# Optimization experiments

Measured on AMD Instinct MI355X. Metric: run time of the kernel, lower is better.

Reference implementation:

```python
import jax, jax.numpy as jnp
import numpy as np

N = 1024        # graph nodes
B = 64          # batch
F_IN = 128
F_OUT = 128
DEG = 8         # avg degree of the random adjacency
NEG = -9.0e15   # mask fill value used by the original module


def _make_masks():
    rng = np.random.default_rng(0)
    a = rng.random((N, N)) < (DEG / N)
    a = np.triu(a, 1)
    adj = (a | a.T).astype(np.float32)          # symmetric, no self loops
    m0 = np.eye(N, dtype=bool)                  # adj_0 = I
    m1 = adj > 0                                # adj_1 = adj
    a2 = adj @ adj
    m2 = a2 > 0                                 # adj_2 = adj @ adj
    a3 = a2 @ adj
    m3 = a3 > 0                                 # adj_3 = adj_2 @ adj
    return m0, m1, m2, m3


def setup_inputs() -> dict:
    key = jax.random.key(0)
    ks = jax.random.split(key, 8)
    m0, m1, m2, m3 = _make_masks()
    return {
        "x": jax.random.normal(ks[0], (B, N, F_IN), dtype=jnp.float32),
        "W": jax.random.normal(ks[1], (4, F_IN, F_OUT), dtype=jnp.float32) * 0.1,
        "E0": jax.random.normal(ks[2], (N, N), dtype=jnp.float32),
        "E1": jax.random.normal(ks[3], (N, N), dtype=jnp.float32),
        "E2": jax.random.normal(ks[4], (N, N), dtype=jnp.float32),
        "E3": jax.random.normal(ks[5], (N, N), dtype=jnp.float32),
        "bias": jax.random.normal(ks[6], (4 * F_OUT,), dtype=jnp.float32) * 0.05,
        "m0": jnp.asarray(m0),
        "m1": jnp.asarray(m1),
        "m2": jnp.asarray(m2),
        "m3": jnp.asarray(m3),
    }


def reference(x, W, E0, E1, E2, E3, bias, m0, m1, m2, m3):
    def hop(E, m, Wk):
        h = jnp.einsum('bnf,fo->bno', x, Wk)                  # [B,N,F_OUT]
        A = jax.nn.softmax(jnp.where(m, E, NEG), axis=1)      # row-softmax over masked scores
        return jnp.einsum('ij,bjo->bio', A, h)                # [B,N,F_OUT]

    out0 = hop(E0, m0, W[0])
    out1 = hop(E1, m1, W[1])
    out2 = hop(E2, m2, W[2])
    out3 = hop(E3, m3, W[3])
    out = jnp.concatenate([out0, out1, out2, out3], axis=2)   # [B,N,4*F_OUT]
    return out + bias[None, None, :]
```

## Files before the change

kernel.cpp:

```cpp
#include <hip/hip_runtime.h>
#include <cstdint>
#include <cstddef>


#define NODES 1024
#define BATCH 64
#define FDIM  128

typedef __attribute__((ext_vector_type(8)))  short  short8;
typedef __attribute__((ext_vector_type(4)))  float  floatx4;
typedef __attribute__((ext_vector_type(16))) float  floatx16;

__device__ __forceinline__ unsigned short f2bf(float f) {
  union { float f; unsigned int u; } v; v.f = f;
  unsigned int r = v.u + 0x7fffu + ((v.u >> 16) & 1u);
  return (unsigned short)(r >> 16);
}

__device__ __forceinline__ void async_copy16(const void* g, void* l) {
  __builtin_amdgcn_global_load_lds(
      (const __attribute__((address_space(1))) void*)g,
      (__attribute__((address_space(3))) void*)l, 16, 0, 0);
}

__device__ __forceinline__ void wg_barrier() {
  asm volatile("" ::: "memory");
  __builtin_amdgcn_s_barrier();
  asm volatile("" ::: "memory");
}

__global__ __launch_bounds__(256) void prep(
    const float* __restrict__ E1, const float* __restrict__ E2, const float* __restrict__ E3,
    const void* __restrict__ m1v, const void* __restrict__ m2v, const void* __restrict__ m3v,
    const void* __restrict__ m0v, unsigned short* __restrict__ Aout,
    const float* __restrict__ W, unsigned short* __restrict__ Wt) {
  const int row = blockIdx.x, hop = blockIdx.y;
  const int tid = threadIdx.x;

  if (hop == 3) {
    if (row < 256) {
      const int idx = row * 256 + tid;
      const int k = idx >> 14, rem = idx & 16383;
      const int f = rem >> 7, o = rem & 127;
      Wt[(k << 14) + o * 128 + f] = f2bf(W[idx]);
    }
    return;
  }

  const int lane = tid & 63, wave = tid >> 6;
  const float* E  = (hop == 0) ? E1 : (hop == 1) ? E2 : E3;
  const void* mv  = (hop == 0) ? m1v : (hop == 1) ? m2v : m3v;
  const bool bytelay = (((const int*)m0v)[256] != 0);

  float v[4]; bool mk[4];
#pragma unroll
  for (int i = 0; i < 4; ++i) {
    const int j = tid + i * 256;
    const size_t e = (size_t)row * NODES + j;
    const bool m = bytelay ? (((const unsigned char*)mv)[e] != 0)
                           : (((const int*)mv)[e] != 0);
    mk[i] = m;
    v[i] = m ? E[e] : -__builtin_inff();
  }
  float mx = fmaxf(fmaxf(v[0], v[1]), fmaxf(v[2], v[3]));
#pragma unroll
  for (int off = 32; off > 0; off >>= 1) mx = fmaxf(mx, __shfl_down(mx, off));
  __shared__ float rm[4], rs[4];
  if (lane == 0) rm[wave] = mx;
  __syncthreads();
  mx = fmaxf(fmaxf(rm[0], rm[1]), fmaxf(rm[2], rm[3]));

  float ex[4], s = 0.f;
#pragma unroll
  for (int i = 0; i < 4; ++i) {
    ex[i] = mk[i] ? __expf(v[i] - mx) : 0.f;
    s += ex[i];
  }
#pragma unroll
  for (int off = 32; off > 0; off >>= 1) s += __shfl_down(s, off);
  if (lane == 0) rs[wave] = s;
  __syncthreads();
  s = rs[0] + rs[1] + rs[2] + rs[3];

  const bool uni = (mx == -__builtin_inff());
  const float inv = uni ? 0.f : 1.f / s;
  unsigned short* dst = Aout + (size_t)hop * NODES * NODES + (size_t)row * NODES;
#pragma unroll
  for (int i = 0; i < 4; ++i) {
    const float val = uni ? (1.f / 1024.f) : ex[i] * inv;
    dst[tid + i * 256] = f2bf(val);
  }
}

__global__ __launch_bounds__(256) void h_gemm(
    const float* __restrict__ x, const unsigned short* __restrict__ Wt,
    const float* __restrict__ bias, unsigned short* __restrict__ Ht,
    float* __restrict__ out) {
  __shared__ unsigned short sX[128 * 128];
  __shared__ unsigned short sW[128 * 128];
  const int jt = blockIdx.x, b = blockIdx.y;
  const int tid = threadIdx.x, lane = tid & 63, wave = tid >> 6;
  const int ln = lane & 15, q = lane >> 4;
  const int p = ln & 7;
  const int j0 = jt * 128;

#pragma unroll
  for (int t = 0; t < 16; ++t) {
    const int g = tid + t * 256;
    const int row = g >> 5, c4 = (g & 31) * 4;
    const float4 vv = *(const float4*)(x + ((size_t)b * NODES + j0 + row) * FDIM + c4);
    ushort4 u;
    u.x = f2bf(vv.x); u.y = f2bf(vv.y); u.z = f2bf(vv.z); u.w = f2bf(vv.w);
    const int col8 = c4 >> 3, off = c4 & 7;
    const int p8 = (col8 & 8) | ((col8 ^ (row & 7)) & 7);
    *(ushort4*)(&sX[row * 128 + p8 * 8 + off]) = u;
  }

  for (int kz = 0; kz < 4; ++kz) {
#pragma unroll
    for (int t = 0; t < 8; ++t) {
      const int gi = wave * 512 + t * 64 + lane;
      const int row = gi >> 4, kb = gi & 15;
      const int src8 = ((kb & 8) | ((kb ^ (row & 7)) & 7)) * 8;
      async_copy16(Wt + (kz << 14) + row * 128 + src8,
                   (char*)sW + (size_t)(wave * 512 + t * 64) * 16);
    }
    __syncthreads();

    const unsigned short* aT = (kz == 0) ? sX : sW;
    const unsigned short* bT = (kz == 0) ? sW : sX;
    floatx4 acc[2][8];
#pragma unroll
    for (int r = 0; r < 2; ++r)
#pragma unroll
      for (int c = 0; c < 8; ++c) acc[r][c] = (floatx4){0.f, 0.f, 0.f, 0.f};

#pragma unroll
    for (int f0 = 0; f0 < 128; f0 += 32) {
      const int cl = (f0 >> 3) + q;
      const int cp = (cl & 8) | ((cl ^ p) & 7);
      short8 af[2], bfr[8];
#pragma unroll
      for (int r = 0; r < 2; ++r)
        af[r] = *(const short8*)(aT + (wave * 32 + r * 16 + ln) * 128 + cp * 8);
#pragma unroll
      for (int c = 0; c < 8; ++c)
        bfr[c] = *(const short8*)(bT + (c * 16 + ln) * 128 + cp * 8);
#pragma unroll
      for (int r = 0; r < 2; ++r)
#pragma unroll
        for (int c = 0; c < 8; ++c)
          acc[r][c] = __builtin_amdgcn_mfma_f32_16x16x32_bf16(af[r], bfr[c], acc[r][c], 0, 0, 0);
    }

    if (kz == 0) {
#pragma unroll
      for (int r = 0; r < 2; ++r)
#pragma unroll
        for (int c = 0; c < 8; ++c) {
          const int o = c * 16 + ln;
          const float bs = bias[o];
#pragma unroll
          for (int reg = 0; reg < 4; ++reg) {
            const int j = j0 + wave * 32 + r * 16 + q * 4 + reg;
            __builtin_nontemporal_store(acc[r][c][reg] + bs,
                                        out + ((size_t)b * NODES + j) * 512 + o);
          }
        }
    } else {
      unsigned short* H = Ht + (size_t)(kz - 1) * 8192 * 1024;
#pragma unroll
      for (int r = 0; r < 2; ++r)
#pragma unroll
        for (int c = 0; c < 8; ++c)
#pragma unroll
          for (int reg = 0; reg < 4; ++reg) {
            const int o = wave * 32 + r * 16 + q * 4 + reg;
            const int j = j0 + c * 16 + ln;
            H[(size_t)(b * 128 + o) * 1024 + j] = f2bf(acc[r][c][reg]);
          }
    }
    __syncthreads();
  }
}

__global__ __launch_bounds__(256, 3) void ah_gemm(
    const unsigned short* __restrict__ Aall, const unsigned short* __restrict__ Htall,
    const float* __restrict__ bias, float* __restrict__ out) {
  __shared__ unsigned short sA[128 * 64];
  __shared__ unsigned short sB[256 * 64];

  const int phys = blockIdx.x;
  const int wid  = (phys & 7) * 96 + (phys >> 3);
  const int hop  = wid >> 8;
  const int r8   = wid & 255;
  const int bm   = r8 & 7;
  const int bn   = r8 >> 3;

  const int tid = threadIdx.x, lane = tid & 63, wave = tid >> 6;
  const int wm = wave >> 1, wn = wave & 1;
  const int l32 = lane & 31, h32 = lane >> 5;
  const int p = l32 & 7;
  const int i0 = bm * 128, n0 = bn * 256;

  const unsigned short* Ab = Aall  + (size_t)hop * NODES * NODES + (size_t)i0 * NODES;
  const unsigned short* Bb = Htall + (size_t)hop * 8192 * 1024   + (size_t)n0 * 1024;

  floatx16 acc[2][4];
#pragma unroll
  for (int r = 0; r < 2; ++r)
#pragma unroll
    for (int c = 0; c < 4; ++c)
#pragma unroll
      for (int e = 0; e < 16; ++e) acc[r][c][e] = 0.f;

  for (int kt = 0; kt < 16; ++kt) {
    const int j0 = kt * 64;
#pragma unroll
    for (int s = 0; s < 4; ++s) {
      const int gi = tid + s * 256;
      const int row = gi >> 3, kb = gi & 7;
      const int src8 = (kb ^ (row & 7)) * 8;
      async_copy16(Ab + (size_t)row * NODES + j0 + src8,
                   (char*)sA + (size_t)gi * 16);
    }
#pragma unroll
    for (int s = 0; s < 8; ++s) {
      const int gi = tid + s * 256;
      const int row = gi >> 3, kb = gi & 7;
      const int src8 = (kb ^ (row & 7)) * 8;
      async_copy16(Bb + (size_t)row * 1024 + j0 + src8,
                   (char*)sB + (size_t)gi * 16);
    }
    __syncthreads();

#pragma unroll
    for (int k0 = 0; k0 < 64; k0 += 16) {
      const int cl = (k0 >> 3) + h32;
      const int cp = cl ^ p;
      short8 af[2], bfr[4];
#pragma unroll
      for (int r = 0; r < 2; ++r)
        af[r] = *(const short8*)(sA + (wm * 64 + r * 32 + l32) * 64 + cp * 8);
#pragma unroll
      for (int c = 0; c < 4; ++c)
        bfr[c] = *(const short8*)(sB + (wn * 128 + c * 32 + l32) * 64 + cp * 8);
#pragma unroll
      for (int r = 0; r < 2; ++r)
#pragma unroll
        for (int c = 0; c < 4; ++c)
          acc[r][c] = __builtin_amdgcn_mfma_f32_32x32x16_bf16(af[r], bfr[c], acc[r][c], 0, 0, 0);
    }
    wg_barrier();
  }

  const int kidx = hop + 1;
  const float* bsl = bias + kidx * 128;
#pragma unroll
  for (int r = 0; r < 2; ++r)
#pragma unroll
    for (int c = 0; c < 4; ++c) {
      const int nn = n0 + wn * 128 + c * 32 + l32;
      const int b = nn >> 7, o = nn & 127;
      const float bv = bsl[o];
#pragma unroll
      for (int reg = 0; reg < 16; ++reg) {
        const int rowin = (reg & 3) + 8 * (reg >> 2) + 4 * h32;
        const int i = i0 + wm * 64 + r * 32 + rowin;
        __builtin_nontemporal_store(acc[r][c][reg] + bv,
            out + ((size_t)b * NODES + i) * 512 + kidx * 128 + o);
      }
    }
}

extern "C" void kernel_launch(void* const* d_in, const int* in_sizes, int n_in,
                              void* d_out, int out_size, void* d_ws, size_t ws_size,
                              hipStream_t stream) {
  (void)in_sizes; (void)n_in; (void)out_size; (void)ws_size;
  const float* x    = (const float*)d_in[0];
  const float* W    = (const float*)d_in[1];
  const float* E1   = (const float*)d_in[3];
  const float* E2   = (const float*)d_in[4];
  const float* E3   = (const float*)d_in[5];
  const float* bias = (const float*)d_in[6];
  const void*  m0   = d_in[7];
  const void*  m1   = d_in[8];
  const void*  m2   = d_in[9];
  const void*  m3   = d_in[10];
  float* out = (float*)d_out;

  unsigned short* Aw  = (unsigned short*)d_ws;
  unsigned short* Htw = Aw + (size_t)3 * NODES * NODES;
  unsigned short* Wtw = Htw + (size_t)3 * 8192 * 1024;

  prep<<<dim3(NODES, 4), 256, 0, stream>>>(E1, E2, E3, m1, m2, m3, m0, Aw, W, Wtw);
  h_gemm<<<dim3(8, BATCH), 256, 0, stream>>>(x, Wtw, bias, Htw, out);
  ah_gemm<<<dim3(768), 256, 0, stream>>>(Aw, Htw, bias, out);
}
```

Baseline: 295.8 us.

## Shrink A·H GEMM tile to 128x128 with 16x16x32 MFMA and plain 3D grid

Reworks the A·H GEMM kernel to use 128x128 output tiles instead of 128x256, with 16x16x32 bf16 MFMAs in place of 32x32x16, and a straightforward 3D grid (batch, row block, hop) that replaces the swizzled 1D block mapping. The smaller LDS footprint and accumulator set are meant to allow higher occupancy, and the launch now has twice as many blocks. In exchange each block reuses its A tile across fewer columns, which raises global and LDS traffic. Dropping the XCD-aware block remapping may also hurt L2 locality.

```diff
diff --git a/kernel.cpp b/kernel.cpp
--- a/kernel.cpp
+++ b/kernel.cpp
@@ -9,7 +9,6 @@
 
 typedef __attribute__((ext_vector_type(8)))  short  short8;
 typedef __attribute__((ext_vector_type(4)))  float  floatx4;
-typedef __attribute__((ext_vector_type(16))) float  floatx16;
 
 __device__ __forceinline__ unsigned short f2bf(float f) {
   union { float f; unsigned int u; } v; v.f = f;
@@ -184,35 +183,28 @@
   }
 }
 
-__global__ __launch_bounds__(256, 3) void ah_gemm(
+__global__ __launch_bounds__(256) void ah_gemm(
     const unsigned short* __restrict__ Aall, const unsigned short* __restrict__ Htall,
     const float* __restrict__ bias, float* __restrict__ out) {
   __shared__ unsigned short sA[128 * 64];
-  __shared__ unsigned short sB[256 * 64];
-
-  const int phys = blockIdx.x;
-  const int wid  = (phys & 7) * 96 + (phys >> 3);
-  const int hop  = wid >> 8;
-  const int r8   = wid & 255;
-  const int bm   = r8 & 7;
-  const int bn   = r8 >> 3;
-
+  __shared__ unsigned short sB[128 * 64];
+  const int bn = blockIdx.x;
+  const int bm = blockIdx.y;
+  const int hop = blockIdx.z;
   const int tid = threadIdx.x, lane = tid & 63, wave = tid >> 6;
   const int wm = wave >> 1, wn = wave & 1;
-  const int l32 = lane & 31, h32 = lane >> 5;
-  const int p = l32 & 7;
-  const int i0 = bm * 128, n0 = bn * 256;
+  const int ln = lane & 15, q = lane >> 4;
+  const int p = ln & 7;
+  const int i0 = bm * 128;
 
   const unsigned short* Ab = Aall  + (size_t)hop * NODES * NODES + (size_t)i0 * NODES;
-  const unsigned short* Bb = Htall + (size_t)hop * 8192 * 1024   + (size_t)n0 * 1024;
-
-  floatx16 acc[2][4];
-#pragma unroll
-  for (int r = 0; r < 2; ++r)
-#pragma unroll
-    for (int c = 0; c < 4; ++c)
-#pragma unroll
-      for (int e = 0; e < 16; ++e) acc[r][c][e] = 0.f;
+  const unsigned short* Bb = Htall + (size_t)hop * 8192 * 1024   + (size_t)bn * 128 * 1024;
+
+  floatx4 acc[4][4];
+#pragma unroll
+  for (int mi = 0; mi < 4; ++mi)
+#pragma unroll
+    for (int ni = 0; ni < 4; ++ni) acc[mi][ni] = (floatx4){0.f, 0.f, 0.f, 0.f};
 
   for (int kt = 0; kt < 16; ++kt) {
     const int j0 = kt * 64;
@@ -225,7 +217,7 @@
                    (char*)sA + (size_t)gi * 16);
     }
 #pragma unroll
-    for (int s = 0; s < 8; ++s) {
+    for (int s = 0; s < 4; ++s) {
       const int gi = tid + s * 256;
       const int row = gi >> 3, kb = gi & 7;
       const int src8 = (kb ^ (row & 7)) * 8;
@@ -235,21 +227,21 @@
     __syncthreads();
 
 #pragma unroll
-    for (int k0 = 0; k0 < 64; k0 += 16) {
-      const int cl = (k0 >> 3) + h32;
-      const int cp = cl ^ p;
-      short8 af[2], bfr[4];
-#pragma unroll
-      for (int r = 0; r < 2; ++r)
-        af[r] = *(const short8*)(sA + (wm * 64 + r * 32 + l32) * 64 + cp * 8);
-#pragma unroll
-      for (int c = 0; c < 4; ++c)
-        bfr[c] = *(const short8*)(sB + (wn * 128 + c * 32 + l32) * 64 + cp * 8);
-#pragma unroll
-      for (int r = 0; r < 2; ++r)
-#pragma unroll
-        for (int c = 0; c < 4; ++c)
-          acc[r][c] = __builtin_amdgcn_mfma_f32_32x32x16_bf16(af[r], bfr[c], acc[r][c], 0, 0, 0);
+    for (int ks = 0; ks < 2; ++ks) {
+      const int cp = (q + ks * 4) ^ p;
+      short8 af[4], bfr[4];
+#pragma unroll
+      for (int mi = 0; mi < 4; ++mi)
+        af[mi] = *(const short8*)(sA + (wm * 64 + mi * 16 + ln) * 64 + cp * 8);
+#pragma unroll
+      for (int ni = 0; ni < 4; ++ni)
+        bfr[ni] = *(const short8*)(sB + (wn * 64 + ni * 16 + ln) * 64 + cp * 8);
+#pragma unroll
+      for (int mi = 0; mi < 4; ++mi)
+#pragma unroll
+        for (int ni = 0; ni < 4; ++ni)
+          acc[mi][ni] = __builtin_amdgcn_mfma_f32_16x16x32_bf16(
+              af[mi], bfr[ni], acc[mi][ni], 0, 0, 0);
     }
     wg_barrier();
   }
@@ -257,19 +249,16 @@
   const int kidx = hop + 1;
   const float* bsl = bias + kidx * 128;
 #pragma unroll
-  for (int r = 0; r < 2; ++r)
-#pragma unroll
-    for (int c = 0; c < 4; ++c) {
-      const int nn = n0 + wn * 128 + c * 32 + l32;
-      const int b = nn >> 7, o = nn & 127;
+  for (int mi = 0; mi < 4; ++mi)
+#pragma unroll
+    for (int ni = 0; ni < 4; ++ni) {
+      const int o = wn * 64 + ni * 16 + ln;
       const float bv = bsl[o];
-#pragma unroll
-      for (int reg = 0; reg < 16; ++reg) {
-        const int rowin = (reg & 3) + 8 * (reg >> 2) + 4 * h32;
-        const int i = i0 + wm * 64 + r * 32 + rowin;
-        __builtin_nontemporal_store(acc[r][c][reg] + bv,
-            out + ((size_t)b * NODES + i) * 512 + kidx * 128 + o);
-      }
+      const int ibase = i0 + wm * 64 + mi * 16 + q * 4;
+#pragma unroll
+      for (int reg = 0; reg < 4; ++reg)
+        __builtin_nontemporal_store(acc[mi][ni][reg] + bv,
+            out + ((size_t)bn * NODES + ibase + reg) * 512 + kidx * 128 + o);
     }
 }
 
@@ -295,5 +284,5 @@
 
   prep<<<dim3(NODES, 4), 256, 0, stream>>>(E1, E2, E3, m1, m2, m3, m0, Aw, W, Wtw);
   h_gemm<<<dim3(8, BATCH), 256, 0, stream>>>(x, Wtw, bias, Htw, out);
-  ah_gemm<<<dim3(768), 256, 0, stream>>>(Aw, Htw, bias, out);
-}
+  ah_gemm<<<dim3(BATCH, 8, 3), 256, 0, stream>>>(Aw, Htw, bias, out);
+}
```

After: 273.2 us. 1.08x faster.
